# Kernel tuning notes

Hardware: AMD Instinct MI355X
Metric: run time of the kernel (lower is better)

Reference implementation:

```python
import jax, jax.numpy as jnp
import numpy as np
from jax import lax

N_BISECT = 32


def setup_inputs() -> dict:
    key = jax.random.key(0)
    k1, k2 = jax.random.split(key)
    B, D = 128, 1024
    N = 512
    x = jax.random.normal(k1, (B, D), dtype=jnp.float32)
    W = jax.random.normal(k2, (N, D), dtype=jnp.float32)
    lam = jnp.float32(0.5)  # positive scalar
    return {"x": x, "W": W, "lam": lam}


def reference(x, W, lam):
    """Moreau-tropical layer forward.

    For each (b, n): z = W[n] + x[b] (length-D vector). Bisect for tau such
    that sum_d relu(z_d - tau) == lam (N_BISECT fixed steps), then
    delta = sum_d relu(z_d - tau)^2 / (2*lam) and y = tau + delta.
    """
    lam32 = lam.astype(jnp.float32)
    # z: [B, N, D] pairwise sums, computed in fp32 like the Triton kernel
    z = x[:, None, :].astype(jnp.float32) + W[None, :, :].astype(jnp.float32)
    tau_lo = jnp.min(z, axis=-1) - lam32          # [B, N]
    tau_hi = jnp.max(z, axis=-1)                  # [B, N]

    def body(_, carry):
        lo, hi = carry
        mid = 0.5 * (lo + hi)
        f = jnp.sum(jnp.maximum(z - mid[..., None], 0.0), axis=-1)  # [B, N]
        too_low = f > lam32
        lo = jnp.where(too_low, mid, lo)
        hi = jnp.where(too_low, hi, mid)
        return lo, hi

    tau_lo, tau_hi = lax.fori_loop(0, N_BISECT, body, (tau_lo, tau_hi))
    tau = 0.5 * (tau_lo + tau_hi)                 # [B, N] fp32
    slack = jnp.maximum(z - tau[..., None], 0.0)  # [B, N, D]
    delta = jnp.sum(slack * slack, axis=-1) / (2.0 * lam32)  # [B, N]
    y = (tau + delta).astype(x.dtype)
    return y
```

## Files before the change

kernel.cpp:

```cpp
#include <hip/hip_runtime.h>


#define D_DIM   1024
#define TBP     8
#define TNP     8
#define NPAIR   64
#define NTHR    256
#define CAPP    32
#define NB      20
#define NEG_INF (-3.0e38f)

__global__ void __launch_bounds__(NTHR, 4)
moreau_tropical(const float* __restrict__ x, const float* __restrict__ W,
                const float* __restrict__ lam_p, float* __restrict__ out,
                int B, int N) {
    __shared__ float cand[CAPP * NPAIR];
    __shared__ float pmax[NPAIR];
    __shared__ int   pcnt[NPAIR];

    const int tid = threadIdx.x;
    const int s   = tid & 31;
    const int bl  = tid >> 5;
    const int b0  = blockIdx.y * TBP;
    const int n0  = blockIdx.x * TNP;
    const float lam = lam_p[0];

    if (tid < NPAIR) pcnt[tid] = 0;
    __syncthreads();

    const float* xg = x + (size_t)min(b0 + bl, B - 1) * D_DIM;
    float4 xr[8];
#pragma unroll
    for (int g = 0; g < 8; ++g) xr[g] = *(const float4*)(xg + g * 128 + s * 4);

    float4 wa[8], wb[8];
    {
        const float* wg = W + (size_t)min(n0, N - 1) * D_DIM;
#pragma unroll
        for (int g = 0; g < 8; ++g) wa[g] = *(const float4*)(wg + g * 128 + s * 4);
    }

#define INS(v, pr)                                                             \
    if ((v) > thr) {                                                           \
        int i_ = atomicAdd(&pcnt[pr], 1);                                      \
        if (i_ < CAPP) cand[i_ * NPAIR + (pr)] = (v);                          \
    }

#define STEP(CUR, NXT, NL)                                                     \
    {                                                                          \
        const int nn = ((NL) + 1 < TNP) ? (NL) + 1 : (NL);                     \
        const float* wg_ = W + (size_t)min(n0 + nn, N - 1) * D_DIM;            \
        _Pragma("unroll")                                                      \
        for (int g = 0; g < 8; ++g)                                            \
            NXT[g] = *(const float4*)(wg_ + g * 128 + s * 4);    \
        float gmax[8];                                                         \
        _Pragma("unroll")                                                      \
        for (int g = 0; g < 8; ++g) {                                          \
            CUR[g].x += xr[g].x; CUR[g].y += xr[g].y;                          \
            CUR[g].z += xr[g].z; CUR[g].w += xr[g].w;                          \
            gmax[g] = fmaxf(fmaxf(CUR[g].x, CUR[g].y),                         \
                            fmaxf(CUR[g].z, CUR[g].w));                        \
        }                                                                      \
        float m_ = gmax[0];                                                    \
        _Pragma("unroll")                                                      \
        for (int g = 1; g < 8; ++g) m_ = fmaxf(m_, gmax[g]);                   \
        _Pragma("unroll")                                                      \
        for (int o = 1; o < 32; o <<= 1)                                       \
            m_ = fmaxf(m_, __shfl_xor(m_, o, 64));     \
        const int pr_ = bl * TNP + (NL);                                       \
        if (s == 0) pmax[pr_] = m_;                                            \
        const float thr = m_ - lam;                                            \
        _Pragma("unroll")                                                      \
        for (int g = 0; g < 8; ++g) {                                          \
            if (gmax[g] > thr) {                                               \
                INS(CUR[g].x, pr_); INS(CUR[g].y, pr_);                        \
                INS(CUR[g].z, pr_); INS(CUR[g].w, pr_);                        \
            }                                                                  \
        }                                                                      \
    }

#pragma unroll 1
    for (int nl = 0; nl < TNP; nl += 2) {
        STEP(wa, wb, nl);
        STEP(wb, wa, nl + 1);
    }
#undef STEP
#undef INS

    __syncthreads();

    if (tid < NPAIR) {
        const int p  = tid;
        const int pb = p >> 3;
        const int pn = p & 7;
        const int K  = pcnt[p];
        const float M   = pmax[p];
        const float thr = M - lam;
        float tau, delta;

        if (K <= CAPP) {
            int Kw = min(K, CAPP);
#pragma unroll
            for (int m = 1; m < 64; m <<= 1) Kw = max(Kw, __shfl_xor(Kw, m, 64));

            float lo = thr, hi = M;
            for (int it = 0; it < NB; ++it) {
                const float mid = 0.5f * (lo + hi);
                float f = 0.0f;
                for (int j = 0; j < Kw; ++j) {
                    float v = cand[j * NPAIR + p];
                    v = (j < K) ? v : NEG_INF;
                    f += fmaxf(v - mid, 0.0f);
                }
                if (f > lam) lo = mid; else hi = mid;
            }
            tau = 0.5f * (lo + hi);
            float s2 = 0.0f;
            for (int j = 0; j < Kw; ++j) {
                float v = cand[j * NPAIR + p];
                v = (j < K) ? v : NEG_INF;
                const float t = fmaxf(v - tau, 0.0f);
                s2 += t * t;
            }
            delta = s2 / (2.0f * lam);
        } else {
            const float* xr_ = x + (size_t)min(b0 + pb, B - 1) * D_DIM;
            const float* wr_ = W + (size_t)min(n0 + pn, N - 1) * D_DIM;
            float lo = thr, hi = M;
            for (int it = 0; it < NB; ++it) {
                const float mid = 0.5f * (lo + hi);
                float f = 0.0f;
                for (int d = 0; d < D_DIM; ++d)
                    f += fmaxf(xr_[d] + wr_[d] - mid, 0.0f);
                if (f > lam) lo = mid; else hi = mid;
            }
            tau = 0.5f * (lo + hi);
            float s2 = 0.0f;
            for (int d = 0; d < D_DIM; ++d) {
                const float t = fmaxf(xr_[d] + wr_[d] - tau, 0.0f);
                s2 += t * t;
            }
            delta = s2 / (2.0f * lam);
        }

        const int ob = min(b0 + pb, B - 1);
        const int on = min(n0 + pn, N - 1);
        out[(size_t)ob * N + on] = tau + delta;
    }
}

extern "C" void kernel_launch(void* const* d_in, const int* in_sizes, int n_in,
                              void* d_out, int out_size, void* d_ws, size_t ws_size,
                              hipStream_t stream) {
    const float* x    = (const float*)d_in[0];
    const float* W    = (const float*)d_in[1];
    const float* lamp = (const float*)d_in[2];
    float* out        = (float*)d_out;

    const int B = in_sizes[0] / D_DIM;
    const int N = in_sizes[1] / D_DIM;

    dim3 grid((N + TNP - 1) / TNP, (B + TBP - 1) / TBP);
    moreau_tropical<<<grid, NTHR, 0, stream>>>(x, W, lamp, out, B, N);
}
```

Before: 82.87 us.

## Map one full wavefront per batch row, shrink tile and bisection steps

Each 64-lane wavefront now covers a whole batch row, using four float4 loads per lane instead of a half-wave using eight. The block tile shrinks from 8x8 to 4x8 pairs, so the grid doubles and the launch-bounds occupancy hint rises from 4 to 8 blocks. The serial candidate bisection drops from 20 to 16 iterations, which cuts the single-lane tail work but leaves tau slightly less precise. The Kw shuffle reduction now spans 32 lanes to match the 32 pairs per block.

```diff
diff --git a/kernel.cpp b/kernel.cpp
--- a/kernel.cpp
+++ b/kernel.cpp
@@ -2,15 +2,15 @@
 
 
 #define D_DIM   1024
-#define TBP     8
-#define TNP     8
-#define NPAIR   64
+#define WB      4
+#define WN      8
+#define NPAIR   32
 #define NTHR    256
 #define CAPP    32
-#define NB      20
+#define NB      16
 #define NEG_INF (-3.0e38f)
 
-__global__ void __launch_bounds__(NTHR, 4)
+__global__ void __launch_bounds__(NTHR, 8)
 moreau_tropical(const float* __restrict__ x, const float* __restrict__ W,
                 const float* __restrict__ lam_p, float* __restrict__ out,
                 int B, int N) {
@@ -18,71 +18,73 @@
     __shared__ float pmax[NPAIR];
     __shared__ int   pcnt[NPAIR];
 
-    const int tid = threadIdx.x;
-    const int s   = tid & 31;
-    const int bl  = tid >> 5;
-    const int b0  = blockIdx.y * TBP;
-    const int n0  = blockIdx.x * TNP;
+    const int tid  = threadIdx.x;
+    const int lane = tid & 63;
+    const int w    = tid >> 6;
+    const int b0   = blockIdx.y * WB;
+    const int n0   = blockIdx.x * WN;
     const float lam = lam_p[0];
 
     if (tid < NPAIR) pcnt[tid] = 0;
     __syncthreads();
 
-    const float* xg = x + (size_t)min(b0 + bl, B - 1) * D_DIM;
-    float4 xr[8];
+    const float* xg = x + (size_t)min(b0 + w, B - 1) * D_DIM + lane * 4;
+    float4 xr[4];
 #pragma unroll
-    for (int g = 0; g < 8; ++g) xr[g] = *(const float4*)(xg + g * 128 + s * 4);
+    for (int g = 0; g < 4; ++g) xr[g] = *(const float4*)(xg + g * 256);
 
-    float4 wa[8], wb[8];
+    float4 wa[4], wb_[4];
     {
-        const float* wg = W + (size_t)min(n0, N - 1) * D_DIM;
+        const float* wg = W + (size_t)min(n0, N - 1) * D_DIM + lane * 4;
 #pragma unroll
-        for (int g = 0; g < 8; ++g) wa[g] = *(const float4*)(wg + g * 128 + s * 4);
+        for (int g = 0; g < 4; ++g) wa[g] = *(const float4*)(wg + g * 256);
     }
 
-#define INS(v, pr)                                                             \
-    if ((v) > thr) {                                                           \
-        int i_ = atomicAdd(&pcnt[pr], 1);                                      \
-        if (i_ < CAPP) cand[i_ * NPAIR + (pr)] = (v);                          \
+#define INS(v)                                                        \
+    if ((v) > thr) {                                                  \
+        int i_ = atomicAdd(&pcnt[pr_], 1);                            \
+        if (i_ < CAPP) cand[i_ * NPAIR + pr_] = (v);                  \
     }
 
-#define STEP(CUR, NXT, NL)                                                     \
-    {                                                                          \
-        const int nn = ((NL) + 1 < TNP) ? (NL) + 1 : (NL);                     \
-        const float* wg_ = W + (size_t)min(n0 + nn, N - 1) * D_DIM;            \
-        _Pragma("unroll")                                                      \
-        for (int g = 0; g < 8; ++g)                                            \
-            NXT[g] = *(const float4*)(wg_ + g * 128 + s * 4);    \
-        float gmax[8];                                                         \
-        _Pragma("unroll")                                                      \
-        for (int g = 0; g < 8; ++g) {                                          \
-            CUR[g].x += xr[g].x; CUR[g].y += xr[g].y;                          \
-            CUR[g].z += xr[g].z; CUR[g].w += xr[g].w;                          \
-            gmax[g] = fmaxf(fmaxf(CUR[g].x, CUR[g].y),                         \
-                            fmaxf(CUR[g].z, CUR[g].w));                        \
-        }                                                                      \
-        float m_ = gmax[0];                                                    \
-        _Pragma("unroll")                                                      \
-        for (int g = 1; g < 8; ++g) m_ = fmaxf(m_, gmax[g]);                   \
-        _Pragma("unroll")                                                      \
-        for (int o = 1; o < 32; o <<= 1)                                       \
-            m_ = fmaxf(m_, __shfl_xor(m_, o, 64));     \
-        const int pr_ = bl * TNP + (NL);                                       \
-        if (s == 0) pmax[pr_] = m_;                                            \
-        const float thr = m_ - lam;                                            \
-        _Pragma("unroll")                                                      \
-        for (int g = 0; g < 8; ++g) {                                          \
-            if (gmax[g] > thr) {                                               \
-                INS(CUR[g].x, pr_); INS(CUR[g].y, pr_);                        \
-                INS(CUR[g].z, pr_); INS(CUR[g].w, pr_);                        \
-            }                                                                  \
-        }                                                                      \
+#define STEP(CUR, NXT, NL)                                                    \
+    {                                                                         \
+        const int nn = ((NL) + 1 < WN) ? (NL) + 1 : (NL);                     \
+        const float* wgn = W + (size_t)min(n0 + nn, N - 1) * D_DIM + lane * 4;\
+        _Pragma("unroll")                                                     \
+        for (int g = 0; g < 4; ++g)                                           \
+            NXT[g] = *(const float4*)(wgn + g * 256);           \
+        float gmax[4];                                                        \
+        _Pragma("unroll")                                                     \
+        for (int g = 0; g < 4; ++g) {                                         \
+            CUR[g].x += xr[g].x; CUR[g].y += xr[g].y;                         \
+            CUR[g].z += xr[g].z; CUR[g].w += xr[g].w;                         \
+            gmax[g] = fmaxf(fmaxf(CUR[g].x, CUR[g].y),                        \
+                            fmaxf(CUR[g].z, CUR[g].w));                       \
+        }                                                                     \
+        const float lmax = fmaxf(fmaxf(gmax[0], gmax[1]),                     \
+                                 fmaxf(gmax[2], gmax[3]));                    \
+        float m_ = lmax;                                                      \
+        _Pragma("unroll")                                                     \
+        for (int o = 1; o < 64; o <<= 1)                                      \
+            m_ = fmaxf(m_, __shfl_xor(m_, o, 64));                            \
+        const int pr_ = w * WN + (NL);                                        \
+        if (lane == 0) pmax[pr_] = m_;                                        \
+        const float thr = m_ - lam;                                           \
+        if (lmax > thr) {                      \
+            _Pragma("unroll")                                                 \
+            for (int g = 0; g < 4; ++g) {                                     \
+                if (gmax[g] > thr) {                                          \
+                    INS(CUR[g].x); INS(CUR[g].y);                             \
+                    INS(CUR[g].z); INS(CUR[g].w);                             \
+                }                                                             \
+            }                                                                 \
+        }                                                                     \
     }
 
 #pragma unroll 1
-    for (int nl = 0; nl < TNP; nl += 2) {
-        STEP(wa, wb, nl);
-        STEP(wb, wa, nl + 1);
+    for (int nl = 0; nl < WN; nl += 2) {
+        STEP(wa, wb_, nl);
+        STEP(wb_, wa, nl + 1);
     }
 #undef STEP
 #undef INS
@@ -99,9 +101,9 @@
         float tau, delta;
 
         if (K <= CAPP) {
-            int Kw = min(K, CAPP);
+            int Kw = K;
 #pragma unroll
-            for (int m = 1; m < 64; m <<= 1) Kw = max(Kw, __shfl_xor(Kw, m, 64));
+            for (int m = 1; m < 32; m <<= 1) Kw = max(Kw, __shfl_xor(Kw, m, 64));
 
             float lo = thr, hi = M;
             for (int it = 0; it < NB; ++it) {
@@ -160,6 +162,6 @@
     const int B = in_sizes[0] / D_DIM;
     const int N = in_sizes[1] / D_DIM;
 
-    dim3 grid((N + TNP - 1) / TNP, (B + TBP - 1) / TBP);
+    dim3 grid((N + WN - 1) / WN, (B + WB - 1) / WB);
     moreau_tropical<<<grid, NTHR, 0, stream>>>(x, W, lamp, out, B, N);
 }
```

After: 80.19 us. -3.2%, faster.
